# Kernel optimization log

Measured on AMD Instinct MI355X. Metric: run time of the kernel, lower is better.

The kernel has to match this reference:

```python
import jax, jax.numpy as jnp
import numpy as np

D_IN, D_ATTN, STEPS = 1024, 64, 2
P_TOP, TAU, LN_EPS = 0.9, 1.0, 1e-5
N = 4096

def _xavier(key, shape):
    fan_in, fan_out = shape[0], shape[1]
    lim = jnp.sqrt(6.0 / (fan_in + fan_out))
    return jax.random.uniform(key, shape, jnp.float32, -lim, lim)

def setup_inputs() -> dict:
    key = jax.random.key(0)
    ks = jax.random.split(key, 12)
    X = jax.random.normal(ks[0], (N, D_IN), jnp.float32)
    S = jax.random.uniform(ks[1], (N, N), jnp.float32)
    # weights stored so that y = x @ W (transposed vs torch nn.Linear.weight)
    W1 = _xavier(ks[2], (D_IN, D_ATTN))
    W3 = _xavier(ks[3], (D_IN, D_ATTN))
    W2 = _xavier(ks[4], (D_ATTN, D_ATTN))  # used raw: Q @ W2 @ K.T
    U1_0 = _xavier(ks[5], (D_IN, D_IN))
    U1_1 = _xavier(ks[6], (D_IN, D_IN))
    U2_0 = _xavier(ks[7], (D_IN, D_IN))
    U2_1 = _xavier(ks[8], (D_IN, D_IN))
    gamma = jnp.ones((D_IN,), jnp.float32)
    beta = jnp.zeros((D_IN,), jnp.float32)
    return {"X": X, "S": S, "W1": W1, "W2": W2, "W3": W3,
            "U1_0": U1_0, "U1_1": U1_1, "U2_0": U2_0, "U2_1": U2_1,
            "gamma": gamma, "beta": beta}

def _adj_from_feats(Xa, W1, W2, W3):
    # bilinear attention logits: (N, N)
    Q = Xa @ W1
    K = Xa @ W3
    logits = (Q @ W2) @ K.T / TAU
    n = logits.shape[1]
    order = jnp.argsort(-logits, axis=1)                       # descending
    vals = jnp.take_along_axis(logits, order, axis=1)
    probs = jax.nn.softmax(vals, axis=1)
    csum = jnp.cumsum(probs, axis=1)
    k_i = jnp.sum(csum < P_TOP, axis=1) + 1                    # per-row top-p count
    keep = jnp.arange(n)[None, :] < k_i[:, None]
    masked_sorted = jnp.where(keep, vals, -jnp.inf)
    rows = jnp.arange(n)[:, None]
    masked = jnp.full_like(logits, -jnp.inf).at[rows, order].set(masked_sorted)
    return jax.nn.softmax(masked, axis=1)

def reference(X, S, W1, W2, W3, U1_0, U1_1, U2_0, U2_1, gamma, beta):
    n = X.shape[0]
    S = S + jnp.eye(n, dtype=X.dtype)
    R = S / jnp.clip(S.sum(axis=1, keepdims=True), 1e-12)      # row-normalized prior
    Z = jnp.zeros_like(X)
    Xf, Xa = X, X
    U1s, U2s = (U1_0, U1_1), (U2_0, U2_1)
    for s in range(STEPS):
        A = _adj_from_feats(Xa, W1, W2, W3)
        Xf = R @ Xf
        Xa = A @ Xa
        Z = Z + (Xf @ U1s[s] + Xa @ U2s[s])                    # dropout = identity (eval)
    Y = X + Z
    mu = Y.mean(axis=-1, keepdims=True)
    var = Y.var(axis=-1, keepdims=True)
    return (Y - mu) * jax.lax.rsqrt(var + LN_EPS) * gamma + beta
```

## Files before the change

### kernel.cpp

```cpp
#include <hip/hip_runtime.h>
#include <cstddef>
#include <cmath>

#define N_TOK 4096
#define D_INF 1024
#define OB_Q 384

typedef unsigned long long u64;
typedef __attribute__((ext_vector_type(8))) short bf16x8;
typedef __attribute__((ext_vector_type(4))) float f32x4;

__device__ __forceinline__ float blockSum(float x, float* red) {
#pragma unroll
  for (int o = 32; o; o >>= 1) x += __shfl_xor(x, o);
  __syncthreads();
  if ((threadIdx.x & 63) == 0) red[threadIdx.x >> 6] = x;
  __syncthreads();
  return (red[0] + red[1]) + (red[2] + red[3]);
}

__device__ __forceinline__ int blockSumI512(int x, int* red) {
#pragma unroll
  for (int o = 32; o; o >>= 1) x += __shfl_xor(x, o);
  __syncthreads();
  if ((threadIdx.x & 63) == 0) red[threadIdx.x >> 6] = x;
  __syncthreads();
  int s = 0;
#pragma unroll
  for (int w = 0; w < 8; ++w) s += red[w];
  return s;
}

__device__ __forceinline__ float np_expf(float x) {
  const float log2e = 1.44269504088896341f;
  float q = __builtin_rintf(x * log2e);
  float r = __builtin_fmaf(q, -0.693359375f, x);
  r = __builtin_fmaf(q, 2.12194440e-4f, r);
  float poly = 1.9875691500e-4f;
  poly = __builtin_fmaf(poly, r, 1.3981999507e-3f);
  poly = __builtin_fmaf(poly, r, 8.3334519073e-3f);
  poly = __builtin_fmaf(poly, r, 4.1665795894e-2f);
  poly = __builtin_fmaf(poly, r, 1.6666665459e-1f);
  poly = __builtin_fmaf(poly, r, 5.0000001201e-1f);
  float zz = r * r;
  poly = __builtin_fmaf(poly, zz, r);
  poly = poly + 1.0f;
  return __builtin_ldexpf(poly, (int)q);
}

__device__ float npPairwiseSum4096(const float* __restrict__ buf, float* share) {
  int t = threadIdx.x;
  __syncthreads();
  if (t < 32) {
    const float* a = buf + (t << 7);
    float r0 = a[0], r1 = a[1], r2 = a[2], r3 = a[3];
    float r4 = a[4], r5 = a[5], r6 = a[6], r7 = a[7];
    for (int i = 8; i < 128; i += 8) {
      r0 += a[i];     r1 += a[i + 1]; r2 += a[i + 2]; r3 += a[i + 3];
      r4 += a[i + 4]; r5 += a[i + 5]; r6 += a[i + 6]; r7 += a[i + 7];
    }
    float leaf = ((r0 + r1) + (r2 + r3)) + ((r4 + r5) + (r6 + r7));
    leaf += __shfl_xor(leaf, 1);
    leaf += __shfl_xor(leaf, 2);
    leaf += __shfl_xor(leaf, 4);
    leaf += __shfl_xor(leaf, 8);
    leaf += __shfl_xor(leaf, 16);
    if (t == 0) share[0] = leaf;
  }
  __syncthreads();
  return share[0];
}

__device__ __forceinline__ unsigned desc_key(float v) {
  unsigned u = __float_as_uint(v);
  unsigned m = (u & 0x80000000u) ? ~u : (u | 0x80000000u);
  return ~m;
}
__device__ __forceinline__ float desc_key_inv(unsigned k) {
  unsigned m = ~k;
  return __uint_as_float((m & 0x80000000u) ? (m ^ 0x80000000u) : ~m);
}

__device__ __forceinline__ unsigned short f2bf(float f) {
  unsigned u = __float_as_uint(f);
  return (unsigned short)((u + 0x7FFFu + ((u >> 16) & 1u)) >> 16);
}

__global__ __launch_bounds__(256) void rowsum_kernel(const float* __restrict__ S,
                                                     float* __restrict__ rs) {
  __shared__ float red[4];
  const float* s = S + (size_t)blockIdx.x * N_TOK;
  float acc = 0.f;
  for (int j = threadIdx.x; j < N_TOK; j += 256) acc += s[j];
  acc = blockSum(acc, red);
  if (threadIdx.x == 0) rs[blockIdx.x] = 1.0f / fmaxf(acc + 1.0f, 1e-12f);
}

__global__ void wcat_kernel(const float* __restrict__ W1,
                            const float* __restrict__ W3, float* __restrict__ Wc) {
  int r = blockIdx.x;
  int c = threadIdx.x;
  Wc[r * 128 + c] = (c < 64) ? W1[r * 64 + c] : W3[r * 64 + (c - 64)];
}

__global__ __launch_bounds__(256) void qw_kernel(const float* __restrict__ QK,
                                                 const float* __restrict__ W2,
                                                 float* __restrict__ QW) {
  __shared__ float w[64][65];
  int t = threadIdx.x;
#pragma unroll
  for (int v = 0; v < 16; ++v) {
    int idx = t + v * 256;
    w[idx >> 6][idx & 63] = W2[idx];
  }
  __syncthreads();
  int row = blockIdx.x * 4 + (t >> 6);
  int c = t & 63;
  const float* q = QK + (size_t)row * 128;
  float acc = 0.f;
#pragma unroll
  for (int k = 0; k < 64; ++k) acc = __builtin_fmaf(q[k], w[k][c], acc);
  QW[(size_t)row * 64 + c] = acc;
}

__device__ __forceinline__ int ob_step(int rem) {
  if (rem >= 2 * OB_Q) return OB_Q;
  if (rem > OB_Q) return ((rem / 2) + 15) & ~15;
  return rem;
}

template <int BETA>
__global__ __launch_bounds__(256) void gemm_tile(const float* __restrict__ A,
                                                 const float* __restrict__ B,
                                                 float* __restrict__ C,
                                                 int M, int N, int K) {
  __shared__ float As[16][68];
  __shared__ float Bs[16][68];
  int t = threadIdx.x;
  int tx = t & 15, ty = t >> 4;
  int row0 = blockIdx.y * 64, col0 = blockIdx.x * 64;
  float tot[4][4] = {};
  float acc[4][4] = {};
  int next_b = ob_step(K);
  for (int k0 = 0; k0 < K; k0 += 16) {
    if (k0 == next_b) {
#pragma unroll
      for (int i = 0; i < 4; ++i)
#pragma unroll
        for (int j = 0; j < 4; ++j) { tot[i][j] += acc[i][j]; acc[i][j] = 0.f; }
      next_b = k0 + ob_step(K - k0);
    }
#pragma unroll
    for (int v = 0; v < 4; ++v) {
      int idx = t + v * 256;
      int r = idx >> 4, c = idx & 15;
      As[c][r] = A[(size_t)(row0 + r) * K + k0 + c];
    }
#pragma unroll
    for (int v = 0; v < 4; ++v) {
      int idx = t + v * 256;
      int r = idx >> 6, c = idx & 63;
      Bs[r][c] = B[(size_t)(k0 + r) * N + col0 + c];
    }
    __syncthreads();
#pragma unroll
    for (int kk = 0; kk < 16; ++kk) {
      float4 a = *(const float4*)&As[kk][ty * 4];
      float4 b = *(const float4*)&Bs[kk][tx * 4];
      float av[4] = {a.x, a.y, a.z, a.w};
      float bv[4] = {b.x, b.y, b.z, b.w};
#pragma unroll
      for (int i = 0; i < 4; ++i)
#pragma unroll
        for (int j = 0; j < 4; ++j)
          acc[i][j] = __builtin_fmaf(av[i], bv[j], acc[i][j]);
    }
    __syncthreads();
  }
#pragma unroll
  for (int i = 0; i < 4; ++i)
#pragma unroll
    for (int j = 0; j < 4; ++j) tot[i][j] += acc[i][j];
#pragma unroll
  for (int i = 0; i < 4; ++i) {
    float* cp = &C[(size_t)(row0 + ty * 4 + i) * N + col0 + tx * 4];
    float4 o;
    if (BETA) {
      float4 old = *(const float4*)cp;
      o.x = old.x + tot[i][0]; o.y = old.y + tot[i][1];
      o.z = old.z + tot[i][2]; o.w = old.w + tot[i][3];
    } else {
      o.x = tot[i][0]; o.y = tot[i][1]; o.z = tot[i][2]; o.w = tot[i][3];
    }
    *(float4*)cp = o;
  }
}

__global__ __launch_bounds__(256) void spmm_exact(const float* __restrict__ A,
                                                  const float* __restrict__ X,
                                                  float* __restrict__ C) {
  __shared__ unsigned short idxs[N_TOK];
  __shared__ int wq[4];
  int t = threadIdx.x;
  int lane = t & 63, w = t >> 6;
  int row = blockIdx.x;
  const float* a = A + (size_t)row * N_TOK;

  int base = t * 16;
  int c0 = 0;
#pragma unroll
  for (int u = 0; u < 16; ++u) c0 += (a[base + u] != 0.f) ? 1 : 0;
  int incl = c0;
#pragma unroll
  for (int d = 1; d < 64; d <<= 1) {
    int up = __shfl_up(incl, d);
    if (lane >= d) incl += up;
  }
  if (lane == 63) wq[w] = incl;
  __syncthreads();
  int off = 0;
  for (int ww = 0; ww < w; ++ww) off += wq[ww];
  int total = wq[0] + wq[1] + wq[2] + wq[3];
  int pos = off + incl - c0;
#pragma unroll
  for (int u = 0; u < 16; ++u)
    if (a[base + u] != 0.f) idxs[pos++] = (unsigned short)(base + u);
  __syncthreads();

  int c = t * 4;
  float acc0 = 0.f, acc1 = 0.f, acc2 = 0.f, acc3 = 0.f;
  float tt0 = 0.f, tt1 = 0.f, tt2 = 0.f, tt3 = 0.f;
  int nb = ob_step(N_TOK);
  for (int q = 0; q < total; ++q) {
    int j = idxs[q];
    while (j >= nb) {
      tt0 += acc0; tt1 += acc1; tt2 += acc2; tt3 += acc3;
      acc0 = acc1 = acc2 = acc3 = 0.f;
      nb += ob_step(N_TOK - nb);
    }
    float av = a[j];
    float4 xv = *(const float4*)&X[(size_t)j * D_INF + c];
    acc0 = __builtin_fmaf(av, xv.x, acc0);
    acc1 = __builtin_fmaf(av, xv.y, acc1);
    acc2 = __builtin_fmaf(av, xv.z, acc2);
    acc3 = __builtin_fmaf(av, xv.w, acc3);
  }
  tt0 += acc0; tt1 += acc1; tt2 += acc2; tt3 += acc3;
  float4 o = {tt0, tt1, tt2, tt3};
  *(float4*)&C[(size_t)row * D_INF + c] = o;
}

template <int BETA>
__global__ __launch_bounds__(256) void gemm_bf16(const float* __restrict__ A,
                                                 const float* __restrict__ B,
                                                 float* __restrict__ C,
                                                 int M, int N, int K) {
  __shared__ unsigned short As[128 * 32];
  __shared__ unsigned short Bs[128 * 32];
  const int t = threadIdx.x;
  const int l = t & 63, w = t >> 6, wr = w >> 1, wc = w & 1;
  const int m0 = blockIdx.y * 128, n0 = blockIdx.x * 128;

  f32x4 acc[4][4];
#pragma unroll
  for (int i = 0; i < 4; ++i)
#pragma unroll
    for (int j = 0; j < 4; ++j)
#pragma unroll
      for (int r = 0; r < 4; ++r) acc[i][j][r] = 0.f;

  const int argp = t >> 3;
  const int acc4 = (t & 7) * 4;
  const int bkb = t >> 5;
  const int bnb = t & 31;

  for (int k0 = 0; k0 < K; k0 += 32) {
#pragma unroll
    for (int u = 0; u < 4; ++u) {
      int row = argp * 4 + u;
      float4 v = *(const float4*)&A[(size_t)(m0 + row) * K + k0 + acc4];
      ushort4 h;
      h.x = f2bf(v.x); h.y = f2bf(v.y); h.z = f2bf(v.z); h.w = f2bf(v.w);
      int idx = (row * 32 + acc4) ^ (((row >> 1) & 3) << 3);
      *(ushort4*)&As[idx] = h;
    }
    {
      float4 r0 = *(const float4*)&B[(size_t)(k0 + bkb * 4 + 0) * N + n0 + bnb * 4];
      float4 r1 = *(const float4*)&B[(size_t)(k0 + bkb * 4 + 1) * N + n0 + bnb * 4];
      float4 r2 = *(const float4*)&B[(size_t)(k0 + bkb * 4 + 2) * N + n0 + bnb * 4];
      float4 r3 = *(const float4*)&B[(size_t)(k0 + bkb * 4 + 3) * N + n0 + bnb * 4];
      float c0[4] = {r0.x, r0.y, r0.z, r0.w};
      float c1[4] = {r1.x, r1.y, r1.z, r1.w};
      float c2[4] = {r2.x, r2.y, r2.z, r2.w};
      float c3[4] = {r3.x, r3.y, r3.z, r3.w};
#pragma unroll
      for (int u = 0; u < 4; ++u) {
        int nrow = bnb * 4 + u;
        ushort4 h;
        h.x = f2bf(c0[u]); h.y = f2bf(c1[u]); h.z = f2bf(c2[u]); h.w = f2bf(c3[u]);
        int idx = (nrow * 32 + bkb * 4) ^ (((nrow >> 1) & 3) << 3);
        *(ushort4*)&Bs[idx] = h;
      }
    }
    __syncthreads();
    bf16x8 af[4], bfv[4];
    const int kseg = (l >> 4) * 8;
#pragma unroll
    for (int fr = 0; fr < 4; ++fr) {
      int row = wr * 64 + fr * 16 + (l & 15);
      int idx = (row * 32 + kseg) ^ (((row >> 1) & 3) << 3);
      af[fr] = *(const bf16x8*)&As[idx];
    }
#pragma unroll
    for (int fc = 0; fc < 4; ++fc) {
      int nrow = wc * 64 + fc * 16 + (l & 15);
      int idx = (nrow * 32 + kseg) ^ (((nrow >> 1) & 3) << 3);
      bfv[fc] = *(const bf16x8*)&Bs[idx];
    }
#pragma unroll
    for (int fr = 0; fr < 4; ++fr)
#pragma unroll
      for (int fc = 0; fc < 4; ++fc)
        acc[fr][fc] = __builtin_amdgcn_mfma_f32_16x16x32_bf16(af[fr], bfv[fc],
                                                              acc[fr][fc], 0, 0, 0);
    __syncthreads();
  }
#pragma unroll
  for (int fr = 0; fr < 4; ++fr) {
#pragma unroll
    for (int fc = 0; fc < 4; ++fc) {
      int rbase = m0 + wr * 64 + fr * 16 + ((l >> 4) << 2);
      int col = n0 + wc * 64 + fc * 16 + (l & 15);
#pragma unroll
      for (int r = 0; r < 4; ++r) {
        size_t off = (size_t)(rbase + r) * N + col;
        float v = acc[fr][fc][r];
        C[off] = BETA ? (C[off] + v) : v;
      }
    }
  }
}

__global__ __launch_bounds__(256) void logits_abt(const float* __restrict__ QW,
                                                  const float* __restrict__ QK,
                                                  float* __restrict__ L) {
  __shared__ float Aq[64][68];
  __shared__ float Bk[64][68];
  int t = threadIdx.x;
  int tx = t & 15, ty = t >> 4;
  int row0 = blockIdx.y * 64, col0 = blockIdx.x * 64;
#pragma unroll
  for (int v = 0; v < 16; ++v) {
    int idx = t + v * 256;
    int c = idx & 63, r = idx >> 6;
    Aq[c][r] = QW[(size_t)(row0 + r) * 64 + c];
    Bk[c][r] = QK[(size_t)(col0 + r) * 128 + 64 + c];
  }
  __syncthreads();
  float acc[4][4] = {};
#pragma unroll
  for (int c0 = 0; c0 < 64; ++c0) {
    float4 a = *(const float4*)&Aq[c0][ty * 4];
    float4 b = *(const float4*)&Bk[c0][tx * 4];
    float av[4] = {a.x, a.y, a.z, a.w};
    float bv[4] = {b.x, b.y, b.z, b.w};
#pragma unroll
    for (int i = 0; i < 4; ++i)
#pragma unroll
      for (int j = 0; j < 4; ++j)
        acc[i][j] = __builtin_fmaf(av[i], bv[j], acc[i][j]);
  }
#pragma unroll
  for (int i = 0; i < 4; ++i) {
    float4 o = {acc[i][0], acc[i][1], acc[i][2], acc[i][3]};
    *(float4*)&L[(size_t)(row0 + ty * 4 + i) * N_TOK + col0 + tx * 4] = o;
  }
}

__global__ __launch_bounds__(512) void topp_exact(float* __restrict__ L) {
  __shared__ unsigned key[N_TOK];
  __shared__ unsigned scr[N_TOK];
  __shared__ int hist[256 * 8];
  __shared__ int wred[8];
  __shared__ float fshare;
  __shared__ float mxs;
  __shared__ int kshare;
  __shared__ int ired[8];

  float* l = L + (size_t)blockIdx.x * N_TOK;
  int t = threadIdx.x;
  int lane = t & 63, w = t >> 6;

  for (int i = t; i < N_TOK; i += 512) key[i] = desc_key(l[i]);
  __syncthreads();

  unsigned* cur = key;
  unsigned* dst = scr;
  for (int pass = 0; pass < 4; ++pass) {
    int s = pass * 8;
    for (int i = t; i < 2048; i += 512) hist[i] = 0;
    __syncthreads();
    for (int it = 0; it < 8; ++it) {
      unsigned k = cur[w * 512 + it * 64 + lane];
      int d = (k >> s) & 255;
      u64 m = ~0ull;
#pragma unroll
      for (int b = 0; b < 8; ++b) {
        u64 bal = __ballot((d >> b) & 1);
        m &= ((d >> b) & 1) ? bal : ~bal;
      }
      int leader = __ffsll(m) - 1;
      if (lane == leader) hist[d * 8 + w] += (int)__popcll(m);
    }
    __syncthreads();
    {
      int i0 = t * 4;
      int a0 = hist[i0], a1 = hist[i0 + 1], a2 = hist[i0 + 2], a3 = hist[i0 + 3];
      int sum = a0 + a1 + a2 + a3;
      int incl = sum;
#pragma unroll
      for (int d = 1; d < 64; d <<= 1) {
        int up = __shfl_up(incl, d);
        if (lane >= d) incl += up;
      }
      if (lane == 63) wred[w] = incl;
      __syncthreads();
      int woff = 0;
      for (int ww = 0; ww < w; ++ww) woff += wred[ww];
      int base = woff + incl - sum;
      hist[i0] = base;
      hist[i0 + 1] = base + a0;
      hist[i0 + 2] = base + a0 + a1;
      hist[i0 + 3] = base + a0 + a1 + a2;
    }
    __syncthreads();
    for (int it = 0; it < 8; ++it) {
      unsigned k = cur[w * 512 + it * 64 + lane];
      int d = (k >> s) & 255;
      u64 m = ~0ull;
#pragma unroll
      for (int b = 0; b < 8; ++b) {
        u64 bal = __ballot((d >> b) & 1);
        m &= ((d >> b) & 1) ? bal : ~bal;
      }
      int leader = __ffsll(m) - 1;
      int old = 0;
      if (lane == leader) {
        old = hist[d * 8 + w];
        hist[d * 8 + w] = old + (int)__popcll(m);
      }
      old = __shfl(old, leader);
      int rank = old + (int)__popcll(m & ((1ull << lane) - 1ull));
      dst[rank] = k;
    }
    __syncthreads();
    unsigned* tmp = cur; cur = dst; dst = tmp;
  }

  float* p = (float*)scr;

  if (t == 0) mxs = desc_key_inv(key[0]);
  __syncthreads();
  float mx = mxs;
  for (int i = t; i < N_TOK; i += 512) p[i] = np_expf(desc_key_inv(key[i]) - mx);
  float tot = npPairwiseSum4096(p, &fshare);

  for (int i = t; i < N_TOK; i += 512) p[i] = p[i] / tot;
  __syncthreads();

  if (t == 0) {
    float c = 0.f;
    int cnt2 = 0;
    for (int j = 0; j < N_TOK; ++j) {
      c += p[j];
      if (c < 0.9f) ++cnt2; else break;
    }
    kshare = (cnt2 + 1 < N_TOK) ? cnt2 + 1 : N_TOK;
  }
  __syncthreads();
  int kcut = kshare;

  unsigned kt = key[kcut - 1];
  int cg = 0, ce = 0;
  for (int i = t; i < N_TOK; i += 512) {
    unsigned kv = key[i];
    cg += (kv < kt) ? 1 : 0;
    ce += (kv == kt) ? 1 : 0;
  }
  cg = blockSumI512(cg, ired);
  ce = blockSumI512(ce, ired);
  int m_keep = kcut - cg;
  bool allties = (m_keep == ce);
  __syncthreads();

  float* sbuf = (float*)scr;

  for (int i = t; i < N_TOK; i += 512) {
    float v = l[i];
    unsigned vk = desc_key(v);
    key[i] = __float_as_uint(v);
    bool keep = allties ? (vk <= kt) : (vk < kt);
    sbuf[i] = keep ? np_expf(v - mx) : 0.f;
  }
  __syncthreads();
  if (!allties && t == 0) {
    int taken = 0;
    for (int i = 0; i < N_TOK && taken < m_keep; ++i) {
      float v = __uint_as_float(key[i]);
      if (desc_key(v) == kt) { sbuf[i] = np_expf(v - mx); ++taken; }
    }
  }
  float denom = npPairwiseSum4096(sbuf, &fshare);

  for (int i = t; i < N_TOK; i += 512) l[i] = sbuf[i] / denom;
}

__global__ __launch_bounds__(256) void xf_update(float* __restrict__ Xf,
                                                 const float* __restrict__ T,
                                                 const float* __restrict__ rs) {
  int idx = blockIdx.x * 256 + threadIdx.x;
  int row = idx >> 8;
  float r = rs[row];
  float4 a = ((const float4*)T)[idx];
  float4 b = ((const float4*)Xf)[idx];
  float4 o;
  o.x = (a.x + b.x) * r; o.y = (a.y + b.y) * r;
  o.z = (a.z + b.z) * r; o.w = (a.w + b.w) * r;
  ((float4*)Xf)[idx] = o;
}

__global__ __launch_bounds__(256) void ln_kernel(const float* __restrict__ X,
                                                 float* __restrict__ out,
                                                 const float* __restrict__ gamma,
                                                 const float* __restrict__ beta) {
  __shared__ float red[4];
  size_t base = (size_t)blockIdx.x * D_INF;
  int t = threadIdx.x;
  float y[4];
  float s = 0.f, ss = 0.f;
#pragma unroll
  for (int i = 0; i < 4; ++i) {
    int c = i * 256 + t;
    y[i] = X[base + c] + out[base + c];
    s += y[i];
    ss += y[i] * y[i];
  }
  s = blockSum(s, red);
  ss = blockSum(ss, red);
  float mean = s * (1.f / 1024.f);
  float var = ss * (1.f / 1024.f) - mean * mean;
  float rstd = rsqrtf(var + 1e-5f);
#pragma unroll
  for (int i = 0; i < 4; ++i) {
    int c = i * 256 + t;
    out[base + c] = (y[i] - mean) * rstd * gamma[c] + beta[c];
  }
}

extern "C" void kernel_launch(void* const* d_in, const int* in_sizes, int n_in,
                              void* d_out, int out_size, void* d_ws, size_t ws_size,
                              hipStream_t stream) {
  const float* X    = (const float*)d_in[0];
  const float* S    = (const float*)d_in[1];
  const float* W1   = (const float*)d_in[2];
  const float* W2   = (const float*)d_in[3];
  const float* W3   = (const float*)d_in[4];
  const float* U1_0 = (const float*)d_in[5];
  const float* U1_1 = (const float*)d_in[6];
  const float* U2_0 = (const float*)d_in[7];
  const float* U2_1 = (const float*)d_in[8];
  const float* gamma = (const float*)d_in[9];
  const float* beta  = (const float*)d_in[10];
  float* Z = (float*)d_out;

  const size_t ND = (size_t)N_TOK * D_INF;
  const size_t NN = (size_t)N_TOK * N_TOK;
  float* Xf  = (float*)d_ws;
  float* Xa0 = Xf  + ND;
  float* Xa1 = Xa0 + ND;
  float* T   = Xa1 + ND;
  float* L   = T   + ND;
  float* QKb = L   + NN;
  float* QWb = QKb + (size_t)N_TOK * 128;
  float* Wc  = QWb + (size_t)N_TOK * 64;
  float* rs  = Wc  + (size_t)D_INF * 128;

  hipMemcpyAsync(Xf, X, ND * sizeof(float), hipMemcpyDeviceToDevice, stream);
  rowsum_kernel<<<N_TOK, 256, 0, stream>>>(S, rs);
  wcat_kernel<<<D_INF, 128, 0, stream>>>(W1, W3, Wc);

  dim3 g128(D_INF / 128, N_TOK / 128);

  gemm_tile<0><<<dim3(2, 64), 256, 0, stream>>>(X, Wc, QKb, N_TOK, 128, D_INF);
  qw_kernel<<<N_TOK / 4, 256, 0, stream>>>(QKb, W2, QWb);
  logits_abt<<<dim3(64, 64), 256, 0, stream>>>(QWb, QKb, L);
  topp_exact<<<N_TOK, 512, 0, stream>>>(L);
  gemm_bf16<0><<<g128, 256, 0, stream>>>(S, Xf, T, N_TOK, D_INF, N_TOK);
  xf_update<<<4096, 256, 0, stream>>>(Xf, T, rs);
  spmm_exact<<<N_TOK, 256, 0, stream>>>(L, X, Xa0);
  gemm_bf16<0><<<g128, 256, 0, stream>>>(Xf, U1_0, Z, N_TOK, D_INF, D_INF);
  gemm_bf16<1><<<g128, 256, 0, stream>>>(Xa0, U2_0, Z, N_TOK, D_INF, D_INF);

  gemm_tile<0><<<dim3(2, 64), 256, 0, stream>>>(Xa0, Wc, QKb, N_TOK, 128, D_INF);
  qw_kernel<<<N_TOK / 4, 256, 0, stream>>>(QKb, W2, QWb);
  logits_abt<<<dim3(64, 64), 256, 0, stream>>>(QWb, QKb, L);
  topp_exact<<<N_TOK, 512, 0, stream>>>(L);
  gemm_bf16<0><<<g128, 256, 0, stream>>>(S, Xf, T, N_TOK, D_INF, N_TOK);
  xf_update<<<4096, 256, 0, stream>>>(Xf, T, rs);
  gemm_bf16<0><<<g128, 256, 0, stream>>>(L, Xa0, Xa1, N_TOK, D_INF, N_TOK);
  gemm_bf16<1><<<g128, 256, 0, stream>>>(Xf, U1_1, Z, N_TOK, D_INF, D_INF);
  gemm_bf16<1><<<g128, 256, 0, stream>>>(Xa1, U2_1, Z, N_TOK, D_INF, D_INF);

  ln_kernel<<<N_TOK, 256, 0, stream>>>(X, Z, gamma, beta);
}
```

Measured before the change: 2.125 ms.

## Cache radix-sort scatter ranks, shrink histograms, and skew softmax buffer to avoid LDS conflicts

The per-row top-p radix sort now computes each element's local rank and digit in the first ballot pass and keeps them in registers. This removes the second ballot-match pass used for scattering. The histogram is stored as 16-bit counters in a warp-major layout, which cuts shared memory and allows a launch-bounds occupancy hint of six blocks. The exp buffers use a rotated index (PIDX) and rotated pairwise-sum reads, so that the 32 summing threads, each striding 128 floats, no longer hit the same LDS bank. The trade-off is higher register pressure from the per-thread key and rank arrays, plus extra index arithmetic.

New measurement: 1.939 ms. 1.1x faster.

```diff
diff --git a/kernel.cpp b/kernel.cpp
--- a/kernel.cpp
+++ b/kernel.cpp
@@ -48,16 +48,24 @@
   return __builtin_ldexpf(poly, (int)q);
 }
 
-__device__ float npPairwiseSum4096(const float* __restrict__ buf, float* share) {
+__device__ __forceinline__ int PIDX(int i) {
+  return (i & ~127) | ((i + (i >> 7)) & 127);
+}
+
+__device__ float npPairwiseSum4096Rot(const float* __restrict__ buf, float* share) {
   int t = threadIdx.x;
   __syncthreads();
   if (t < 32) {
     const float* a = buf + (t << 7);
-    float r0 = a[0], r1 = a[1], r2 = a[2], r3 = a[3];
-    float r4 = a[4], r5 = a[5], r6 = a[6], r7 = a[7];
+    float r0 = a[t & 127], r1 = a[(t + 1) & 127], r2 = a[(t + 2) & 127],
+          r3 = a[(t + 3) & 127];
+    float r4 = a[(t + 4) & 127], r5 = a[(t + 5) & 127], r6 = a[(t + 6) & 127],
+          r7 = a[(t + 7) & 127];
     for (int i = 8; i < 128; i += 8) {
-      r0 += a[i];     r1 += a[i + 1]; r2 += a[i + 2]; r3 += a[i + 3];
-      r4 += a[i + 4]; r5 += a[i + 5]; r6 += a[i + 6]; r7 += a[i + 7];
+      r0 += a[(i + 0 + t) & 127]; r1 += a[(i + 1 + t) & 127];
+      r2 += a[(i + 2 + t) & 127]; r3 += a[(i + 3 + t) & 127];
+      r4 += a[(i + 4 + t) & 127]; r5 += a[(i + 5 + t) & 127];
+      r6 += a[(i + 6 + t) & 127]; r7 += a[(i + 7 + t) & 127];
     }
     float leaf = ((r0 + r1) + (r2 + r3)) + ((r4 + r5) + (r6 + r7));
     leaf += __shfl_xor(leaf, 1);
@@ -79,6 +87,16 @@
 __device__ __forceinline__ float desc_key_inv(unsigned k) {
   unsigned m = ~k;
   return __uint_as_float((m & 0x80000000u) ? (m ^ 0x80000000u) : ~m);
+}
+
+__device__ __forceinline__ u64 ballot_match8(int d) {
+  u64 m = ~0ull;
+#pragma unroll
+  for (int b = 0; b < 8; ++b) {
+    u64 bal = __ballot((d >> b) & 1);
+    m &= ((d >> b) & 1) ? bal : ~bal;
+  }
+  return m;
 }
 
 __device__ __forceinline__ unsigned short f2bf(float f) {
@@ -377,10 +395,10 @@
   }
 }
 
-__global__ __launch_bounds__(512) void topp_exact(float* __restrict__ L) {
+__global__ __launch_bounds__(512, 6) void topp_exact(float* __restrict__ L) {
   __shared__ unsigned key[N_TOK];
   __shared__ unsigned scr[N_TOK];
-  __shared__ int hist[256 * 8];
+  __shared__ unsigned short hist[8 * 256];
   __shared__ int wred[8];
   __shared__ float fshare;
   __shared__ float mxs;
@@ -390,6 +408,7 @@
   float* l = L + (size_t)blockIdx.x * N_TOK;
   int t = threadIdx.x;
   int lane = t & 63, w = t >> 6;
+  u64 below = (lane == 63) ? 0x7FFFFFFFFFFFFFFFull : ((1ull << lane) - 1ull);
 
   for (int i = t; i < N_TOK; i += 512) key[i] = desc_key(l[i]);
   __syncthreads();
@@ -398,25 +417,33 @@
   unsigned* dst = scr;
   for (int pass = 0; pass < 4; ++pass) {
     int s = pass * 8;
-    for (int i = t; i < 2048; i += 512) hist[i] = 0;
-    __syncthreads();
+    for (int i = t; i < 1024; i += 512) ((int*)hist)[i] = 0;
+    __syncthreads();
+    unsigned myk[8], mypk[8];
+#pragma unroll
     for (int it = 0; it < 8; ++it) {
       unsigned k = cur[w * 512 + it * 64 + lane];
       int d = (k >> s) & 255;
-      u64 m = ~0ull;
-#pragma unroll
-      for (int b = 0; b < 8; ++b) {
-        u64 bal = __ballot((d >> b) & 1);
-        m &= ((d >> b) & 1) ? bal : ~bal;
+      u64 m = ballot_match8(d);
+      int leader = __ffsll(m) - 1;
+      int before = (int)__popcll(m & below);
+      int old = 0;
+      if (lane == leader) {
+        old = (int)hist[w * 256 + d];
+        hist[w * 256 + d] = (unsigned short)(old + (int)__popcll(m));
       }
-      int leader = __ffsll(m) - 1;
-      if (lane == leader) hist[d * 8 + w] += (int)__popcll(m);
+      old = __shfl(old, leader);
+      myk[it] = k;
+      mypk[it] = ((unsigned)(old + before) << 8) | (unsigned)d;
     }
     __syncthreads();
     {
-      int i0 = t * 4;
-      int a0 = hist[i0], a1 = hist[i0 + 1], a2 = hist[i0 + 2], a3 = hist[i0 + 3];
-      int sum = a0 + a1 + a2 + a3;
+      int li = t * 4;
+      int v0 = hist[((li + 0) & 7) * 256 + ((li + 0) >> 3)];
+      int v1 = hist[((li + 1) & 7) * 256 + ((li + 1) >> 3)];
+      int v2 = hist[((li + 2) & 7) * 256 + ((li + 2) >> 3)];
+      int v3 = hist[((li + 3) & 7) * 256 + ((li + 3) >> 3)];
+      int sum = v0 + v1 + v2 + v3;
       int incl = sum;
 #pragma unroll
       for (int d = 1; d < 64; d <<= 1) {
@@ -428,30 +455,18 @@
       int woff = 0;
       for (int ww = 0; ww < w; ++ww) woff += wred[ww];
       int base = woff + incl - sum;
-      hist[i0] = base;
-      hist[i0 + 1] = base + a0;
-      hist[i0 + 2] = base + a0 + a1;
-      hist[i0 + 3] = base + a0 + a1 + a2;
-    }
-    __syncthreads();
+      hist[((li + 0) & 7) * 256 + ((li + 0) >> 3)] = (unsigned short)base;
+      hist[((li + 1) & 7) * 256 + ((li + 1) >> 3)] = (unsigned short)(base + v0);
+      hist[((li + 2) & 7) * 256 + ((li + 2) >> 3)] = (unsigned short)(base + v0 + v1);
+      hist[((li + 3) & 7) * 256 + ((li + 3) >> 3)] =
+          (unsigned short)(base + v0 + v1 + v2);
+    }
+    __syncthreads();
+#pragma unroll
     for (int it = 0; it < 8; ++it) {
-      unsigned k = cur[w * 512 + it * 64 + lane];
-      int d = (k >> s) & 255;
-      u64 m = ~0ull;
-#pragma unroll
-      for (int b = 0; b < 8; ++b) {
-        u64 bal = __ballot((d >> b) & 1);
-        m &= ((d >> b) & 1) ? bal : ~bal;
-      }
-      int leader = __ffsll(m) - 1;
-      int old = 0;
-      if (lane == leader) {
-        old = hist[d * 8 + w];
-        hist[d * 8 + w] = old + (int)__popcll(m);
-      }
-      old = __shfl(old, leader);
-      int rank = old + (int)__popcll(m & ((1ull << lane) - 1ull));
-      dst[rank] = k;
+      int d = mypk[it] & 255;
+      int rank = (int)hist[w * 256 + d] + (int)(mypk[it] >> 8);
+      dst[rank] = myk[it];
     }
     __syncthreads();
     unsigned* tmp = cur; cur = dst; dst = tmp;
@@ -462,17 +477,18 @@
   if (t == 0) mxs = desc_key_inv(key[0]);
   __syncthreads();
   float mx = mxs;
-  for (int i = t; i < N_TOK; i += 512) p[i] = np_expf(desc_key_inv(key[i]) - mx);
-  float tot = npPairwiseSum4096(p, &fshare);
-
-  for (int i = t; i < N_TOK; i += 512) p[i] = p[i] / tot;
+  for (int i = t; i < N_TOK; i += 512)
+    p[PIDX(i)] = np_expf(desc_key_inv(key[i]) - mx);
+  float tot = npPairwiseSum4096Rot(p, &fshare);
+
+  for (int i = t; i < N_TOK; i += 512) p[PIDX(i)] = p[PIDX(i)] / tot;
   __syncthreads();
 
   if (t == 0) {
     float c = 0.f;
     int cnt2 = 0;
     for (int j = 0; j < N_TOK; ++j) {
-      c += p[j];
+      c += p[PIDX(j)];
       if (c < 0.9f) ++cnt2; else break;
     }
     kshare = (cnt2 + 1 < N_TOK) ? cnt2 + 1 : N_TOK;
@@ -500,19 +516,19 @@
     unsigned vk = desc_key(v);
     key[i] = __float_as_uint(v);
     bool keep = allties ? (vk <= kt) : (vk < kt);
-    sbuf[i] = keep ? np_expf(v - mx) : 0.f;
+    sbuf[PIDX(i)] = keep ? np_expf(v - mx) : 0.f;
   }
   __syncthreads();
   if (!allties && t == 0) {
     int taken = 0;
     for (int i = 0; i < N_TOK && taken < m_keep; ++i) {
       float v = __uint_as_float(key[i]);
-      if (desc_key(v) == kt) { sbuf[i] = np_expf(v - mx); ++taken; }
-    }
-  }
-  float denom = npPairwiseSum4096(sbuf, &fshare);
-
-  for (int i = t; i < N_TOK; i += 512) l[i] = sbuf[i] / denom;
+      if (desc_key(v) == kt) { sbuf[PIDX(i)] = np_expf(v - mx); ++taken; }
+    }
+  }
+  float denom = npPairwiseSum4096Rot(sbuf, &fshare);
+
+  for (int i = t; i < N_TOK; i += 512) l[i] = sbuf[PIDX(i)] / denom;
 }
 
 __global__ __launch_bounds__(256) void xf_update(float* __restrict__ Xf,
```
